# Kernel optimization log

Hardware: AMD Instinct MI355X
Metric: run time of the kernel (lower is better)

Reference implementation:

```python
import jax, jax.numpy as jnp
import numpy as np


def setup_inputs() -> dict:
    key = jax.random.key(0)
    k1, k2, k3 = jax.random.split(key, 3)
    B, S, D_IN, D_OUT = 4, 2048, 4096, 4096
    x = jax.random.normal(k1, (B, S, D_IN), dtype=jnp.float32)
    # int8 quantized weight, stored as int8 (values in [-127, 127])
    weight = jax.random.randint(k2, (D_OUT, D_IN), -127, 128, dtype=jnp.int8)
    weight_scaler = jax.random.uniform(k3, (D_OUT,), dtype=jnp.float32) * 0.02
    return {"x": x, "weight": weight, "weight_scaler": weight_scaler}


def reference(x, weight, weight_scaler):
    # quant path: dequantize weight with per-output-channel scale, then F.linear
    w = weight.astype(jnp.float32) * weight_scaler[:, None]  # [D_OUT, D_IN]
    # F.linear(x, w) == x @ w.T
    return jnp.einsum('bsd,od->bso', x, w)
```

## Files before the change

### kernel.cpp

```cpp
#include <hip/hip_runtime.h>
#include <cstdint>
#include <cstddef>

typedef int i32x4 __attribute__((ext_vector_type(4)));

__global__ __launch_bounds__(256) void prep_kernel(
    const float* __restrict__ x, signed char* __restrict__ xq, float* __restrict__ xs,
    const int* __restrict__ w, signed char* __restrict__ wq,
    int K, int xrows) {
  const int t = threadIdx.x;
  if ((int)blockIdx.x < xrows) {
    const int row = blockIdx.x;
    const float4* xr = (const float4*)(x + (size_t)row * K);
    const int n4 = K >> 2;
    float amax = 0.f;
    for (int i = t; i < n4; i += 256) {
      float4 v = xr[i];
      amax = fmaxf(amax, fmaxf(fmaxf(fabsf(v.x), fabsf(v.y)),
                               fmaxf(fabsf(v.z), fabsf(v.w))));
    }
#pragma unroll
    for (int off = 32; off > 0; off >>= 1)
      amax = fmaxf(amax, __shfl_xor(amax, off, 64));
    __shared__ float wmax[4];
    if ((t & 63) == 0) wmax[t >> 6] = amax;
    __syncthreads();
    amax = fmaxf(fmaxf(wmax[0], wmax[1]), fmaxf(wmax[2], wmax[3]));
    const float inv = (amax > 0.f) ? 127.f / amax : 0.f;
    if (t == 0) xs[row] = amax / 127.f;
    int* o = (int*)(xq + (size_t)row * K);
    for (int i = t; i < n4; i += 256) {
      float4 v = xr[i];
      int a = __float2int_rn(v.x * inv) & 0xFF;
      int b = __float2int_rn(v.y * inv) & 0xFF;
      int c = __float2int_rn(v.z * inv) & 0xFF;
      int d = __float2int_rn(v.w * inv) & 0xFF;
      o[i] = a | (b << 8) | (c << 16) | (d << 24);
    }
  } else {
    const size_t g = (size_t)(blockIdx.x - xrows) * 256 + t;
    int4 v = ((const int4*)w)[g];
    ((int*)wq)[g] = (v.x & 0xFF) | ((v.y & 0xFF) << 8) |
                    ((v.z & 0xFF) << 16) | ((v.w & 0xFF) << 24);
  }
}

static __device__ __forceinline__ void gld_lds16(const void* g, void* l) {
  __builtin_amdgcn_global_load_lds(
      (const __attribute__((address_space(1))) unsigned int*)g,
      (__attribute__((address_space(3))) unsigned int*)l,
      16, 0, 0);
}

__global__ __launch_bounds__(512, 2) void gemm_i8_8ph(
    const signed char* __restrict__ A,
    const signed char* __restrict__ B,
    const float* __restrict__ xs,
    const float* __restrict__ ws,
    float* __restrict__ C,
    int M, int N, int K) {
  __shared__ __align__(16) signed char lds[131072];

  const int tid  = threadIdx.x;
  const int lane = tid & 63;
  const int wave = tid >> 6;
  const int wm   = wave >> 2;
  const int wn   = wave & 3;
  const int q    = lane >> 4;
  const int r16  = lane & 15;
  const int e    = lane & 7;

  const int m0 = blockIdx.y << 8;
  const int n0 = blockIdx.x << 8;
  const int NT  = K >> 7;
  const int NT4 = NT << 2;

  const int srow   = tid >> 3;
  const int schunk = ((tid & 7) ^ (srow & 7)) << 4;
  const signed char* sA = A + (size_t)(m0 + srow) * K + schunk;
  const signed char* sB = B + (size_t)(n0 + srow) * K + schunk;
  signed char* lW = lds + wave * 1024;

  const int aro = ((wm << 4) + r16) << 7;
  const int bro = r16 << 7;
  const int cs  = (q ^ e) << 4;

  i32x4 acc[8][4];
#pragma unroll
  for (int i = 0; i < 8; ++i)
#pragma unroll
    for (int j = 0; j < 4; ++j) acc[i][j] = (i32x4){0, 0, 0, 0};
  i32x4 af[4][2], bf[2][2];

#define STAGE(Gv)                                                            \
  do {                                                                       \
    const int G_ = (Gv);                                                     \
    if (G_ < NT4) {                                                          \
      const int t_ = G_ >> 2;                                                \
      const int half_ = (G_ >> 1) & 1;                                       \
      signed char* l_ = lW + ((t_ & 1) << 15) + ((G_ & 1) << 16) +           \
                        (half_ << 14);                                       \
      const signed char* g_ = ((G_ & 1) ? sB : sA) +                         \
                              (size_t)(half_ << 7) * K + ((size_t)t_ << 7);  \
      gld_lds16(g_, l_);                                                     \
      gld_lds16(g_ + (size_t)64 * K, l_ + 8192);                             \
    }                                                                        \
  } while (0)

#define PHASE(MH, NH, READA, Gv, VMW)                                        \
  do {                                                                       \
    if (READA) {                                                             \
      _Pragma("unroll") for (int i_ = 0; i_ < 4; ++i_)                       \
        _Pragma("unroll") for (int kh_ = 0; kh_ < 2; ++kh_)                  \
          af[i_][kh_] = *(const i32x4*)(pA + ((((MH) << 2) + i_) << 12) +    \
                                        aro + (cs ^ (kh_ << 6)));            \
    }                                                                        \
    _Pragma("unroll") for (int j_ = 0; j_ < 2; ++j_)                         \
      _Pragma("unroll") for (int kh_ = 0; kh_ < 2; ++kh_)                    \
        bf[j_][kh_] = *(const i32x4*)(pB + ((NH) << 14) + (wn << 12) +       \
                                      (j_ << 11) + bro + (cs ^ (kh_ << 6))); \
    STAGE(Gv);                                                               \
    __builtin_amdgcn_s_barrier();                                            \
    asm volatile("s_waitcnt lgkmcnt(0)" ::: "memory");                       \
    __builtin_amdgcn_s_setprio(1);                                           \
    _Pragma("unroll") for (int kh_ = 0; kh_ < 2; ++kh_)                      \
      _Pragma("unroll") for (int i_ = 0; i_ < 4; ++i_)                       \
        _Pragma("unroll") for (int j_ = 0; j_ < 2; ++j_)                     \
          acc[((MH) << 2) + i_][((NH) << 1) + j_] =                          \
              __builtin_amdgcn_mfma_i32_16x16x64_i8(                         \
                  af[i_][kh_], bf[j_][kh_],                                  \
                  acc[((MH) << 2) + i_][((NH) << 1) + j_], 0, 0, 0);         \
    __builtin_amdgcn_s_setprio(0);                                           \
    if (VMW) asm volatile("s_waitcnt vmcnt(4)" ::: "memory");                \
    __builtin_amdgcn_s_barrier();                                            \
  } while (0)

  STAGE(0); STAGE(1); STAGE(2); STAGE(3); STAGE(4); STAGE(5);
  asm volatile("s_waitcnt vmcnt(4)" ::: "memory");
  __builtin_amdgcn_s_barrier();

  for (int t = 0; t < NT; ++t) {
    const signed char* pA = lds + ((t & 1) << 15);
    const signed char* pB = lds + 65536 + ((t & 1) << 15);
    const int G0 = t << 2;
    PHASE(0, 0, 1, G0 + 6, 0);
    PHASE(0, 1, 0, G0 + 7, 0);
    PHASE(1, 0, 1, G0 + 8, 0);
    PHASE(1, 1, 0, G0 + 9, 1);
  }
#undef PHASE
#undef STAGE

#pragma unroll
  for (int mt = 0; mt < 8; ++mt) {
    const int row0 = m0 + (mt << 5) + (wm << 4) + (q << 2);
    float xv[4];
#pragma unroll
    for (int r = 0; r < 4; ++r) xv[r] = xs[row0 + r];
#pragma unroll
    for (int nt = 0; nt < 4; ++nt) {
      const int col = n0 + ((nt >> 1) << 7) + (wn << 5) + ((nt & 1) << 4) + r16;
      const float s = ws[col];
      float* Cp = C + (size_t)row0 * N + col;
#pragma unroll
      for (int r = 0; r < 4; ++r)
        Cp[(size_t)r * N] = (float)acc[mt][nt][r] * xv[r] * s;
    }
  }
}

__global__ void naive_kernel(const float* __restrict__ x, const int* __restrict__ w,
                             const float* __restrict__ sc, float* __restrict__ out,
                             int M, int N, int K) {
  int idx = blockIdx.x * 256 + threadIdx.x;
  if (idx >= M * N) return;
  int m = idx / N, n = idx % N;
  const float* xr = x + (size_t)m * K;
  const int*   wr = w + (size_t)n * K;
  float acc = 0.f;
  for (int k = 0; k < K; ++k) acc += xr[k] * (float)wr[k];
  out[idx] = acc * sc[n];
}

extern "C" void kernel_launch(void* const* d_in, const int* in_sizes, int n_in,
                              void* d_out, int out_size, void* d_ws, size_t ws_size,
                              hipStream_t stream) {
  const float* x  = (const float*)d_in[0];
  const int*   w  = (const int*)d_in[1];
  const float* sc = (const float*)d_in[2];
  float* out = (float*)d_out;

  const int N = in_sizes[2];
  const int K = in_sizes[1] / N;
  const int M = in_sizes[0] / K;

  const size_t need = (size_t)M * K + (size_t)N * K + (size_t)M * 4 + 16;
  if (ws_size < need || (M & 255) || (N & 255) || (K & 127) || K < 256 ||
      (((size_t)N * K) % 1024)) {
    int total = M * N;
    naive_kernel<<<(total + 255) / 256, 256, 0, stream>>>(x, w, sc, out, M, N, K);
    return;
  }

  signed char* xq = (signed char*)d_ws;
  signed char* wq = xq + (size_t)M * K;
  float*       xsc = (float*)(wq + (size_t)N * K);

  const int wblocks = (int)(((size_t)N * K) / 1024);
  prep_kernel<<<M + wblocks, 256, 0, stream>>>(x, xq, xsc, w, wq, K, M);

  dim3 grid(N >> 8, M >> 8);
  gemm_i8_8ph<<<grid, 512, 0, stream>>>(xq, wq, xsc, sc, out, M, N, K);
}
```

Baseline: 389.8 us.

## Restructure int8 GEMM main loop into two phases with XCD block remap

```diff
diff --git a/kernel.cpp b/kernel.cpp
--- a/kernel.cpp
+++ b/kernel.cpp
@@ -3,6 +3,14 @@
 #include <cstddef>
 
 typedef int i32x4 __attribute__((ext_vector_type(4)));
+
+static __device__ __forceinline__ int pack4(float4 v, float inv) {
+  int a = __float2int_rn(v.x * inv) & 0xFF;
+  int b = __float2int_rn(v.y * inv) & 0xFF;
+  int c = __float2int_rn(v.z * inv) & 0xFF;
+  int d = __float2int_rn(v.w * inv) & 0xFF;
+  return a | (b << 8) | (c << 16) | (d << 24);
+}
 
 __global__ __launch_bounds__(256) void prep_kernel(
     const float* __restrict__ x, signed char* __restrict__ xq, float* __restrict__ xs,
@@ -13,29 +21,50 @@
     const int row = blockIdx.x;
     const float4* xr = (const float4*)(x + (size_t)row * K);
     const int n4 = K >> 2;
-    float amax = 0.f;
-    for (int i = t; i < n4; i += 256) {
-      float4 v = xr[i];
-      amax = fmaxf(amax, fmaxf(fmaxf(fabsf(v.x), fabsf(v.y)),
-                               fmaxf(fabsf(v.z), fabsf(v.w))));
-    }
-#pragma unroll
-    for (int off = 32; off > 0; off >>= 1)
-      amax = fmaxf(amax, __shfl_xor(amax, off, 64));
     __shared__ float wmax[4];
-    if ((t & 63) == 0) wmax[t >> 6] = amax;
-    __syncthreads();
-    amax = fmaxf(fmaxf(wmax[0], wmax[1]), fmaxf(wmax[2], wmax[3]));
-    const float inv = (amax > 0.f) ? 127.f / amax : 0.f;
-    if (t == 0) xs[row] = amax / 127.f;
-    int* o = (int*)(xq + (size_t)row * K);
-    for (int i = t; i < n4; i += 256) {
-      float4 v = xr[i];
-      int a = __float2int_rn(v.x * inv) & 0xFF;
-      int b = __float2int_rn(v.y * inv) & 0xFF;
-      int c = __float2int_rn(v.z * inv) & 0xFF;
-      int d = __float2int_rn(v.w * inv) & 0xFF;
-      o[i] = a | (b << 8) | (c << 16) | (d << 24);
+    if (n4 == 1024) {
+      float4 v0 = xr[t], v1 = xr[t + 256], v2 = xr[t + 512], v3 = xr[t + 768];
+      float amax = fmaxf(fmaxf(fabsf(v0.x), fabsf(v0.y)),
+                         fmaxf(fabsf(v0.z), fabsf(v0.w)));
+      amax = fmaxf(amax, fmaxf(fmaxf(fabsf(v1.x), fabsf(v1.y)),
+                               fmaxf(fabsf(v1.z), fabsf(v1.w))));
+      amax = fmaxf(amax, fmaxf(fmaxf(fabsf(v2.x), fabsf(v2.y)),
+                               fmaxf(fabsf(v2.z), fabsf(v2.w))));
+      amax = fmaxf(amax, fmaxf(fmaxf(fabsf(v3.x), fabsf(v3.y)),
+                               fmaxf(fabsf(v3.z), fabsf(v3.w))));
+#pragma unroll
+      for (int off = 32; off > 0; off >>= 1)
+        amax = fmaxf(amax, __shfl_xor(amax, off, 64));
+      if ((t & 63) == 0) wmax[t >> 6] = amax;
+      __syncthreads();
+      amax = fmaxf(fmaxf(wmax[0], wmax[1]), fmaxf(wmax[2], wmax[3]));
+      const float inv = (amax > 0.f) ? 127.f / amax : 0.f;
+      if (t == 0) xs[row] = amax / 127.f;
+      int* o = (int*)(xq + (size_t)row * K);
+      o[t]       = pack4(v0, inv);
+      o[t + 256] = pack4(v1, inv);
+      o[t + 512] = pack4(v2, inv);
+      o[t + 768] = pack4(v3, inv);
+    } else {
+      float amax = 0.f;
+      for (int i = t; i < n4; i += 256) {
+        float4 v = xr[i];
+        amax = fmaxf(amax, fmaxf(fmaxf(fabsf(v.x), fabsf(v.y)),
+                                 fmaxf(fabsf(v.z), fabsf(v.w))));
+      }
+#pragma unroll
+      for (int off = 32; off > 0; off >>= 1)
+        amax = fmaxf(amax, __shfl_xor(amax, off, 64));
+      if ((t & 63) == 0) wmax[t >> 6] = amax;
+      __syncthreads();
+      amax = fmaxf(fmaxf(wmax[0], wmax[1]), fmaxf(wmax[2], wmax[3]));
+      const float inv = (amax > 0.f) ? 127.f / amax : 0.f;
+      if (t == 0) xs[row] = amax / 127.f;
+      int* o = (int*)(xq + (size_t)row * K);
+      for (int i = t; i < n4; i += 256) {
+        float4 v = xr[i];
+        o[i] = pack4(v, inv);
+      }
     }
   } else {
     const size_t g = (size_t)(blockIdx.x - xrows) * 256 + t;
@@ -52,7 +81,7 @@
       16, 0, 0);
 }
 
-__global__ __launch_bounds__(512, 2) void gemm_i8_8ph(
+__global__ __launch_bounds__(512, 2) void gemm_i8_2ph(
     const signed char* __restrict__ A,
     const signed char* __restrict__ B,
     const float* __restrict__ xs,
@@ -70,10 +99,13 @@
   const int r16  = lane & 15;
   const int e    = lane & 7;
 
-  const int m0 = blockIdx.y << 8;
-  const int n0 = blockIdx.x << 8;
-  const int NT  = K >> 7;
-  const int NT4 = NT << 2;
+  const unsigned nwg = gridDim.x * gridDim.y;
+  unsigned id = blockIdx.y * gridDim.x + blockIdx.x;
+  if ((nwg & 7u) == 0u) id = (id & 7u) * (nwg >> 3) + (id >> 3);
+  const int m0 = (int)(id / gridDim.x) << 8;
+  const int n0 = (int)(id % gridDim.x) << 8;
+
+  const int NT = K >> 7;
 
   const int srow   = tid >> 3;
   const int schunk = ((tid & 7) ^ (srow & 7)) << 4;
@@ -90,65 +122,73 @@
   for (int i = 0; i < 8; ++i)
 #pragma unroll
     for (int j = 0; j < 4; ++j) acc[i][j] = (i32x4){0, 0, 0, 0};
-  i32x4 af[4][2], bf[2][2];
-
-#define STAGE(Gv)                                                            \
+  i32x4 af[4][2], bf[2][2][2];
+
+#define STAGE(Tv, Gv)                                                        \
   do {                                                                       \
-    const int G_ = (Gv);                                                     \
-    if (G_ < NT4) {                                                          \
-      const int t_ = G_ >> 2;                                                \
-      const int half_ = (G_ >> 1) & 1;                                       \
-      signed char* l_ = lW + ((t_ & 1) << 15) + ((G_ & 1) << 16) +           \
-                        (half_ << 14);                                       \
-      const signed char* g_ = ((G_ & 1) ? sB : sA) +                         \
+    const int t_ = (Tv);                                                     \
+    if (t_ < NT) {                                                           \
+      const int mat_ = (Gv) & 1, half_ = (Gv) >> 1;                          \
+      signed char* l_ = lW + ((t_ & 1) << 15) + (mat_ << 16) + (half_ << 14);\
+      const signed char* g_ = (mat_ ? sB : sA) +                             \
                               (size_t)(half_ << 7) * K + ((size_t)t_ << 7);  \
       gld_lds16(g_, l_);                                                     \
       gld_lds16(g_ + (size_t)64 * K, l_ + 8192);                             \
     }                                                                        \
   } while (0)
 
-#define PHASE(MH, NH, READA, Gv, VMW)                                        \
-  do {                                                                       \
-    if (READA) {                                                             \
-      _Pragma("unroll") for (int i_ = 0; i_ < 4; ++i_)                       \
-        _Pragma("unroll") for (int kh_ = 0; kh_ < 2; ++kh_)                  \
-          af[i_][kh_] = *(const i32x4*)(pA + ((((MH) << 2) + i_) << 12) +    \
-                                        aro + (cs ^ (kh_ << 6)));            \
-    }                                                                        \
+#define READ_A(MH)                                                           \
+  _Pragma("unroll") for (int i_ = 0; i_ < 4; ++i_)                           \
+    _Pragma("unroll") for (int kh_ = 0; kh_ < 2; ++kh_)                      \
+      af[i_][kh_] = *(const i32x4*)(pA + ((((MH) << 2) + i_) << 12) + aro +  \
+                                    (cs ^ (kh_ << 6)));
+
+#define READ_B                                                               \
+  _Pragma("unroll") for (int nh_ = 0; nh_ < 2; ++nh_)                        \
     _Pragma("unroll") for (int j_ = 0; j_ < 2; ++j_)                         \
       _Pragma("unroll") for (int kh_ = 0; kh_ < 2; ++kh_)                    \
-        bf[j_][kh_] = *(const i32x4*)(pB + ((NH) << 14) + (wn << 12) +       \
-                                      (j_ << 11) + bro + (cs ^ (kh_ << 6))); \
-    STAGE(Gv);                                                               \
-    __builtin_amdgcn_s_barrier();                                            \
-    asm volatile("s_waitcnt lgkmcnt(0)" ::: "memory");                       \
-    __builtin_amdgcn_s_setprio(1);                                           \
-    _Pragma("unroll") for (int kh_ = 0; kh_ < 2; ++kh_)                      \
-      _Pragma("unroll") for (int i_ = 0; i_ < 4; ++i_)                       \
+        bf[nh_][j_][kh_] = *(const i32x4*)(pB + (nh_ << 14) + (wn << 12) +   \
+                                           (j_ << 11) + bro + (cs ^ (kh_ << 6)));
+
+#define MFMA_HALF(MH)                                                        \
+  __builtin_amdgcn_s_setprio(1);                                             \
+  _Pragma("unroll") for (int kh_ = 0; kh_ < 2; ++kh_)                        \
+    _Pragma("unroll") for (int i_ = 0; i_ < 4; ++i_)                         \
+      _Pragma("unroll") for (int nh_ = 0; nh_ < 2; ++nh_)                    \
         _Pragma("unroll") for (int j_ = 0; j_ < 2; ++j_)                     \
-          acc[((MH) << 2) + i_][((NH) << 1) + j_] =                          \
+          acc[((MH) << 2) + i_][(nh_ << 1) + j_] =                           \
               __builtin_amdgcn_mfma_i32_16x16x64_i8(                         \
-                  af[i_][kh_], bf[j_][kh_],                                  \
-                  acc[((MH) << 2) + i_][((NH) << 1) + j_], 0, 0, 0);         \
-    __builtin_amdgcn_s_setprio(0);                                           \
-    if (VMW) asm volatile("s_waitcnt vmcnt(4)" ::: "memory");                \
-    __builtin_amdgcn_s_barrier();                                            \
-  } while (0)
-
-  STAGE(0); STAGE(1); STAGE(2); STAGE(3); STAGE(4); STAGE(5);
+                  af[i_][kh_], bf[nh_][j_][kh_],                             \
+                  acc[((MH) << 2) + i_][(nh_ << 1) + j_], 0, 0, 0);          \
+  __builtin_amdgcn_s_setprio(0);
+
+  STAGE(0, 0); STAGE(0, 1); STAGE(0, 2); STAGE(0, 3);
+  STAGE(1, 0); STAGE(1, 1);
   asm volatile("s_waitcnt vmcnt(4)" ::: "memory");
   __builtin_amdgcn_s_barrier();
 
   for (int t = 0; t < NT; ++t) {
     const signed char* pA = lds + ((t & 1) << 15);
     const signed char* pB = lds + 65536 + ((t & 1) << 15);
-    const int G0 = t << 2;
-    PHASE(0, 0, 1, G0 + 6, 0);
-    PHASE(0, 1, 0, G0 + 7, 0);
-    PHASE(1, 0, 1, G0 + 8, 0);
-    PHASE(1, 1, 0, G0 + 9, 1);
-  }
-#undef PHASE
+    READ_A(0);
+    READ_B;
+    STAGE(t + 1, 2); STAGE(t + 1, 3);
+    __builtin_amdgcn_s_barrier();
+    asm volatile("s_waitcnt lgkmcnt(0)" ::: "memory");
+    MFMA_HALF(0);
+    __builtin_amdgcn_s_barrier();
+    READ_A(1);
+    STAGE(t + 2, 0); STAGE(t + 2, 1);
+    __builtin_amdgcn_s_barrier();
+    asm volatile("s_waitcnt lgkmcnt(0)" ::: "memory");
+    MFMA_HALF(1);
+    if (t < NT - 2) asm volatile("s_waitcnt vmcnt(4)" ::: "memory");
+    else            asm volatile("s_waitcnt vmcnt(0)" ::: "memory");
+    __builtin_amdgcn_s_barrier();
+  }
+#undef MFMA_HALF
+#undef READ_B
+#undef READ_A
 #undef STAGE
 
 #pragma unroll
@@ -210,5 +250,5 @@
   prep_kernel<<<M + wblocks, 256, 0, stream>>>(x, xq, xsc, w, wq, K, M);
 
   dim3 grid(N >> 8, M >> 8);
-  gemm_i8_8ph<<<grid, 512, 0, stream>>>(xq, wq, xsc, sc, out, M, N, K);
-}
+  gemm_i8_2ph<<<grid, 512, 0, stream>>>(xq, wq, xsc, sc, out, M, N, K);
+}
```

Result: no change. 383.6 us (-1.6%).
